# Performance work log

Measured on AMD Instinct MI355X. Metric: run time of the kernel, lower is better.

The kernel has to match this reference:

```python
import jax, jax.numpy as jnp
import numpy as np

B, C, H, W = 4, 128, 64, 64
CQK = C // 8


def setup_inputs() -> dict:
    key = jax.random.key(0)
    ks = jax.random.split(key, 8)
    s = 0.02
    return {
        "x": jax.random.normal(ks[0], (B, C, H, W), dtype=jnp.float32),
        "Wq": jax.random.normal(ks[1], (CQK, C), dtype=jnp.float32) * s,
        "bq": jnp.zeros((CQK,), dtype=jnp.float32),
        "Wk": jax.random.normal(ks[2], (CQK, C), dtype=jnp.float32) * s,
        "bk": jnp.zeros((CQK,), dtype=jnp.float32),
        "Wv": jax.random.normal(ks[3], (C, C), dtype=jnp.float32) * s,
        "bv": jnp.zeros((C,), dtype=jnp.float32),
        "gamma": jnp.zeros((1,), dtype=jnp.float32),
    }


def reference(x, Wq, bq, Wk, bk, Wv, bv, gamma):
    b, c, h, w = x.shape
    xf = x.reshape(b, c, h * w)                      # [b, c, n]
    # 1x1 convs == per-position channel matmuls
    q = jnp.einsum('dc,bcn->bdn', Wq, xf) + bq[None, :, None]   # [b, c/8, n]
    k = jnp.einsum('dc,bcn->bdn', Wk, xf) + bk[None, :, None]   # [b, c/8, n]
    v = jnp.einsum('ec,bcn->ben', Wv, xf) + bv[None, :, None]   # [b, c, n]
    energy = jnp.einsum('bdi,bdj->bij', q, k)        # [b, n, n]
    attn = jax.nn.softmax(energy, axis=-1)           # softmax over keys j
    out = jnp.einsum('bcj,bij->bci', v, attn)        # [b, c, n]
    out = out.reshape(b, c, h, w)
    return gamma[0] * out + x
```

## Files before the change

### kernel.cpp

```cpp
#include <hip/hip_runtime.h>
#include <hip/hip_bf16.h>


#define BN 4
#define CC 128
#define NN 4096
#define DQK 16
#define KVB 64

typedef float f32x16 __attribute__((ext_vector_type(16)));
typedef short s16x8 __attribute__((ext_vector_type(8)));
typedef unsigned short u16;

union FragU { unsigned u[4]; s16x8 v; };

#if defined(__has_builtin)
#  if __has_builtin(__builtin_amdgcn_permlane32_swap)
#    define PLSWAP 1
#  endif
#endif

__device__ inline u16 to_bf16(float f) {
  unsigned u = __builtin_bit_cast(unsigned, f);
  unsigned r = u + 0x7fffu + ((u >> 16) & 1u);
  return (u16)(r >> 16);
}
__device__ inline unsigned cvt_pk(float lo, float hi) {
  unsigned r;
  asm("v_cvt_pk_bf16_f32 %0, %1, %2" : "=v"(r) : "v"(lo), "v"(hi));
  return r;
}
__device__ inline float bf16lo_f(unsigned u) {
  return __builtin_bit_cast(float, u << 16);
}
__device__ inline float bf16hi_f(unsigned u) {
  return __builtin_bit_cast(float, u & 0xffff0000u);
}

__device__ inline void half_swap(unsigned& a, unsigned& b) {
#ifdef PLSWAP
  auto r = __builtin_amdgcn_permlane32_swap(a, b, false, false);
  a = r[0]; b = r[1];
#else
  unsigned xa = (unsigned)__shfl_xor((int)a, 32);
  unsigned xb = (unsigned)__shfl_xor((int)b, 32);
  bool hi = (threadIdx.x & 32) != 0;
  unsigned na = hi ? xb : a;
  unsigned nb = hi ? b : xa;
  a = na; b = nb;
#endif
}
__device__ inline float max_partner(float t) {
#ifdef PLSWAP
  unsigned u = __builtin_bit_cast(unsigned, t);
  auto r = __builtin_amdgcn_permlane32_swap(u, u, false, false);
  return fmaxf(__builtin_bit_cast(float, r[0]), __builtin_bit_cast(float, r[1]));
#else
  return fmaxf(t, __shfl_xor(t, 32));
#endif
}
__device__ inline float add_partner(float t) {
#ifdef PLSWAP
  unsigned u = __builtin_bit_cast(unsigned, t);
  auto r = __builtin_amdgcn_permlane32_swap(u, u, false, false);
  return __builtin_bit_cast(float, r[0]) + __builtin_bit_cast(float, r[1]);
#else
  return t + __shfl_xor(t, 32);
#endif
}

__global__ __launch_bounds__(640) void proj_kernel(
    const float* __restrict__ x,
    const float* __restrict__ Wq, const float* __restrict__ bq,
    const float* __restrict__ Wk, const float* __restrict__ bk,
    const float* __restrict__ Wv, const float* __restrict__ bv,
    u16* __restrict__ Qt, u16* __restrict__ Kt, u16* __restrict__ Vb)
{
  __shared__ float xs[CC][64];
  __shared__ u16 vout[CC][64];
  __shared__ u16 qkout[2][32][32];
  const int tid = threadIdx.x;
  const int wave = tid >> 6;
  const int lane = tid & 63;
  const int l31 = lane & 31, h = lane >> 5;
  const int b = blockIdx.x >> 6;
  const int n0 = (blockIdx.x & 63) << 6;

  const float* xb = x + ((size_t)b * CC) * NN + n0;
  #pragma unroll
  for (int k = 0; k < 4; ++k) {
    int id = tid + 640 * k;
    if (id < 2048) {
      int c = id >> 4, f = (id & 15) * 4;
      *reinterpret_cast<float4*>(&xs[c][f]) =
          *reinterpret_cast<const float4*>(xb + (size_t)c * NN + f);
    }
  }
  __syncthreads();

  const int nh = wave & 1, at = wave >> 1;
  const int nc = nh * 32 + l31;

  s16x8 bx[8];
  #pragma unroll
  for (int ks = 0; ks < 8; ++ks) {
    FragU f;
    #pragma unroll
    for (int q = 0; q < 4; ++q) {
      int c = 16 * ks + 8 * h + 2 * q;
      f.u[q] = cvt_pk(xs[c][nc], xs[c + 1][nc]);
    }
    bx[ks] = f.v;
  }

  f32x16 acc;
  #pragma unroll
  for (int r = 0; r < 16; ++r) acc[r] = 0.f;

  const float LOG2E = 1.44269504088896340736f;

  const float* wrow;
  if (at == 0)
    wrow = (l31 < 16) ? (Wq + (size_t)l31 * CC) : (Wk + (size_t)(l31 - 16) * CC);
  else
    wrow = Wv + (size_t)((at - 1) * 32 + l31) * CC;

  #pragma unroll
  for (int ks = 0; ks < 8; ++ks) {
    const float* wp = wrow + 16 * ks + 8 * h;
    float4 w0 = *reinterpret_cast<const float4*>(wp);
    float4 w1 = *reinterpret_cast<const float4*>(wp + 4);
    FragU a;
    a.u[0] = cvt_pk(w0.x, w0.y); a.u[1] = cvt_pk(w0.z, w0.w);
    a.u[2] = cvt_pk(w1.x, w1.y); a.u[3] = cvt_pk(w1.z, w1.w);
    acc = __builtin_amdgcn_mfma_f32_32x32x16_bf16(a.v, bx[ks], acc, 0, 0, 0);
  }

  if (at == 0) {
    #pragma unroll
    for (int r = 0; r < 16; ++r) {
      int row = (r & 3) + 8 * (r >> 2) + 4 * h;
      float val = acc[r];
      val = (row < 16) ? (val + bq[row]) * LOG2E : (val + bk[row - 16]);
      qkout[nh][row][l31] = to_bf16(val);
    }
  } else {
    #pragma unroll
    for (int r = 0; r < 16; ++r) {
      int e = (at - 1) * 32 + (r & 3) + 8 * (r >> 2) + 4 * h;
      vout[e][nh * 32 + l31] = to_bf16(acc[r] + bv[e]);
    }
  }
  __syncthreads();

  for (int id = tid; id < 1024; id += 640) {
    int isK = id >> 9, j = id & 511;
    int ni = j >> 3, ch = j & 7;
    int nhh = ni >> 5, n32 = ni & 31;
    unsigned lo = qkout[nhh][isK * 16 + 2 * ch][n32];
    unsigned hi = qkout[nhh][isK * 16 + 2 * ch + 1][n32];
    u16* dst = (isK ? Kt : Qt) + ((size_t)b * NN + n0 + ni) * DQK + 2 * ch;
    *reinterpret_cast<unsigned*>(dst) = lo | (hi << 16);
  }
  for (int id = tid; id < 1024; id += 640) {
    int c = id >> 3, q16 = id & 7;
    s16x8 v = *reinterpret_cast<const s16x8*>(&vout[c][q16 * 8]);
    *reinterpret_cast<s16x8*>(Vb + ((size_t)b * CC + c) * NN + n0 + q16 * 8) = v;
  }
}

__global__ __launch_bounds__(512, 4) void flash_kernel(
    const u16* __restrict__ Qt, const u16* __restrict__ Kt,
    const u16* __restrict__ Vb,
    unsigned* __restrict__ Opart, float* __restrict__ mstat,
    float* __restrict__ lstat, int JS)
{
  __shared__ u16 Vs[2][CC * KVB];
  __shared__ u16 Ks[2][KVB * DQK];
  const int tid = threadIdx.x;
  const int wv = tid >> 6;
  const int lane = tid & 63;
  const int l31 = lane & 31, h = lane >> 5;
  const int qb = blockIdx.x & 15;
  const int bs = blockIdx.x >> 4;
  const int b = bs / JS, sg = bs % JS;
  const int i0 = qb * 256 + wv * 32;
  const int seglen = NN / JS;
  const int j_begin = sg * seglen;
  const int niter = seglen / KVB;

  const int sc0 = tid >> 3;
  const int so = (tid & 7) * 16;
  const int sw0 = (sc0 & 7) << 4;

  const u16* Kb = Kt + (size_t)b * NN * DQK;
  const u16* Vbb = Vb + (size_t)b * CC * NN;

  const int kp_row = tid >> 1, kp_half = tid & 1;
  const int kp_slot = kp_row * DQK + ((kp_half ^ (kp_row & 1)) << 3);

  s16x8 qf = *reinterpret_cast<const s16x8*>(
      Qt + ((size_t)b * NN + i0 + l31) * DQK + 8 * h);

  f32x16 zero;
  #pragma unroll
  for (int r = 0; r < 16; ++r) zero[r] = 0.f;
  f32x16 acc[4];
  #pragma unroll
  for (int ct = 0; ct < 4; ++ct) acc[ct] = zero;
  float m_run = -__builtin_inff();
  float l_run = 0.f;

  {
    s16x8 g0 = *reinterpret_cast<const s16x8*>(
        Vbb + (size_t)sc0 * NN + j_begin + so / 2);
    s16x8 g1 = *reinterpret_cast<const s16x8*>(
        Vbb + (size_t)(64 + sc0) * NN + j_begin + so / 2);
    *reinterpret_cast<s16x8*>(&Vs[0][sc0 * KVB + ((so ^ sw0) >> 1)]) = g0;
    *reinterpret_cast<s16x8*>(&Vs[0][(64 + sc0) * KVB + ((so ^ sw0) >> 1)]) = g1;
    if (tid < 128) {
      s16x8 gk = *reinterpret_cast<const s16x8*>(
          Kb + (size_t)j_begin * DQK + tid * 8);
      *reinterpret_cast<s16x8*>(&Ks[0][kp_slot]) = gk;
    }
  }
  __syncthreads();

  const int rsw = (l31 & 7) << 4;
  const int kr0 = l31 * DQK + ((h ^ (l31 & 1)) << 3);
  const int kr1 = (32 + l31) * DQK + ((h ^ (l31 & 1)) << 3);

  for (int t = 0; t < niter; ++t) {
    const int cur = t & 1;
    s16x8 g0, g1, gk;
    const bool more = (t + 1 < niter);
    if (more) {
      const int jn = j_begin + (t + 1) * KVB;
      g0 = *reinterpret_cast<const s16x8*>(
          Vbb + (size_t)sc0 * NN + jn + so / 2);
      g1 = *reinterpret_cast<const s16x8*>(
          Vbb + (size_t)(64 + sc0) * NN + jn + so / 2);
      if (tid < 128)
        gk = *reinterpret_cast<const s16x8*>(
            Kb + (size_t)jn * DQK + tid * 8);
    }

    s16x8 kf0 = *reinterpret_cast<const s16x8*>(&Ks[cur][kr0]);
    s16x8 kf1 = *reinterpret_cast<const s16x8*>(&Ks[cur][kr1]);

    #pragma unroll
    for (int s = 0; s < 2; ++s) {
      f32x16 sv = __builtin_amdgcn_mfma_f32_32x32x16_bf16(
          s ? kf1 : kf0, qf, zero, 0, 0, 0);

      float t0 = fmaxf(fmaxf(sv[0], sv[1]), sv[2]);
      float t1 = fmaxf(fmaxf(sv[3], sv[4]), sv[5]);
      float t2 = fmaxf(fmaxf(sv[6], sv[7]), sv[8]);
      float t3 = fmaxf(fmaxf(sv[9], sv[10]), sv[11]);
      float t4 = fmaxf(fmaxf(sv[12], sv[13]), sv[14]);
      float u0 = fmaxf(fmaxf(t0, t1), t2);
      float u1 = fmaxf(fmaxf(t3, t4), sv[15]);
      float cmb = max_partner(fmaxf(u0, u1));
      float m_new = (cmb > m_run + 8.f) ? cmb : m_run;
      if (__any(m_new > m_run)) {
        float alpha = __builtin_amdgcn_exp2f(m_run - m_new);
        l_run *= alpha;
        #pragma unroll
        for (int ct = 0; ct < 4; ++ct)
          #pragma unroll
          for (int r = 0; r < 16; ++r) acc[ct][r] *= alpha;
        m_run = m_new;
      }

      float p[16];
      #pragma unroll
      for (int r = 0; r < 16; ++r)
        p[r] = __builtin_amdgcn_exp2f(sv[r] - m_run);
      float s01 = p[0] + p[1],  s23 = p[2] + p[3];
      float s45 = p[4] + p[5],  s67 = p[6] + p[7];
      float s89 = p[8] + p[9],  sab = p[10] + p[11];
      float scd = p[12] + p[13], sef = p[14] + p[15];
      l_run += ((s01 + s23) + (s45 + s67)) + ((s89 + sab) + (scd + sef));

      unsigned w0_ = cvt_pk(p[0], p[1]),  w1_ = cvt_pk(p[2], p[3]);
      unsigned w2_ = cvt_pk(p[4], p[5]),  w3_ = cvt_pk(p[6], p[7]);
      unsigned w4_ = cvt_pk(p[8], p[9]),  w5_ = cvt_pk(p[10], p[11]);
      unsigned w6_ = cvt_pk(p[12], p[13]), w7_ = cvt_pk(p[14], p[15]);
      half_swap(w0_, w2_);
      half_swap(w1_, w3_);
      half_swap(w4_, w6_);
      half_swap(w5_, w7_);
      FragU f0, f1;
      f0.u[0] = w0_; f0.u[1] = w1_; f0.u[2] = w2_; f0.u[3] = w3_;
      f1.u[0] = w4_; f1.u[1] = w5_; f1.u[2] = w6_; f1.u[3] = w7_;

      #pragma unroll
      for (int ct = 0; ct < 4; ++ct) {
        const int c = 32 * ct + l31;
        s16x8 va = *reinterpret_cast<const s16x8*>(
            &Vs[cur][c * KVB + (((s * 64 + h * 16) ^ rsw) >> 1)]);
        s16x8 vb2 = *reinterpret_cast<const s16x8*>(
            &Vs[cur][c * KVB + (((s * 64 + 32 + h * 16) ^ rsw) >> 1)]);
        acc[ct] = __builtin_amdgcn_mfma_f32_32x32x16_bf16(va, f0.v,
                                                          acc[ct], 0, 0, 0);
        acc[ct] = __builtin_amdgcn_mfma_f32_32x32x16_bf16(vb2, f1.v,
                                                          acc[ct], 0, 0, 0);
      }
    }

    if (more) {
      *reinterpret_cast<s16x8*>(
          &Vs[cur ^ 1][sc0 * KVB + ((so ^ sw0) >> 1)]) = g0;
      *reinterpret_cast<s16x8*>(
          &Vs[cur ^ 1][(64 + sc0) * KVB + ((so ^ sw0) >> 1)]) = g1;
      if (tid < 128)
        *reinterpret_cast<s16x8*>(&Ks[cur ^ 1][kp_slot]) = gk;
    }
    __syncthreads();
  }

  float l_tot = add_partner(l_run);

  unsigned* Ob = Opart + ((size_t)(b * JS + sg) * 64) * NN;
  #pragma unroll
  for (int ct = 0; ct < 4; ++ct)
    #pragma unroll
    for (int q = 0; q < 8; ++q) {
      unsigned pv = cvt_pk(acc[ct][2 * q], acc[ct][2 * q + 1]);
      int c = 32 * ct + ((2 * q) & 3) + 8 * (q >> 1) + 4 * h;
      Ob[(size_t)(c >> 1) * NN + i0 + l31] = pv;
    }
  if (lane < 32) {
    mstat[((size_t)(b * JS + sg)) * NN + i0 + l31] = m_run;
    lstat[((size_t)(b * JS + sg)) * NN + i0 + l31] = l_tot;
  }
}

template <int JS>
__global__ __launch_bounds__(256) void merge_kernel(
    const unsigned* __restrict__ Opart, const float* __restrict__ mstat,
    const float* __restrict__ lstat, const float* __restrict__ x,
    const float* __restrict__ gamma, float* __restrict__ out)
{
  const int tid = threadIdx.x;
  const int il = tid & 63;
  const int cg = tid >> 6;
  const int bid = blockIdx.x;
  const int b = bid >> 8;
  const int rem = bid & 255;
  const int i = (((rem >> 3) << 6) + il) * 2;
  const int c2 = ((rem & 7) * 4 + cg) * 2;

  float m0 = -__builtin_inff(), m1 = m0;
  float ms0[JS], ms1[JS];
  #pragma unroll
  for (int s = 0; s < JS; ++s) {
    const float* mp = mstat + ((size_t)(b * JS + s)) * NN + i;
    ms0[s] = mp[0]; ms1[s] = mp[1];
    m0 = fmaxf(m0, ms0[s]); m1 = fmaxf(m1, ms1[s]);
  }
  float d0 = 0.f, d1 = 0.f;
  float w0[JS], w1[JS];
  #pragma unroll
  for (int s = 0; s < JS; ++s) {
    const float* lp = lstat + ((size_t)(b * JS + s)) * NN + i;
    w0[s] = __builtin_amdgcn_exp2f(ms0[s] - m0);
    w1[s] = __builtin_amdgcn_exp2f(ms1[s] - m1);
    d0 += w0[s] * lp[0];
    d1 += w1[s] * lp[1];
  }
  const float g = gamma[0];
  const float g0 = g / d0, g1 = g / d1;
  #pragma unroll
  for (int s = 0; s < JS; ++s) { w0[s] *= g0; w1[s] *= g1; }

  float o[4][2] = {{0.f, 0.f}, {0.f, 0.f}, {0.f, 0.f}, {0.f, 0.f}};
  #pragma unroll
  for (int s = 0; s < JS; ++s) {
    const unsigned* Ob = Opart + ((size_t)(b * JS + s) * 64) * NN;
    uint2 A = *reinterpret_cast<const uint2*>(&Ob[(size_t)c2 * NN + i]);
    uint2 Bv = *reinterpret_cast<const uint2*>(&Ob[(size_t)(c2 + 1) * NN + i]);
    o[0][0] += w0[s] * bf16lo_f(A.x);  o[1][0] += w0[s] * bf16hi_f(A.x);
    o[0][1] += w1[s] * bf16lo_f(A.y);  o[1][1] += w1[s] * bf16hi_f(A.y);
    o[2][0] += w0[s] * bf16lo_f(Bv.x); o[3][0] += w0[s] * bf16hi_f(Bv.x);
    o[2][1] += w1[s] * bf16lo_f(Bv.y); o[3][1] += w1[s] * bf16hi_f(Bv.y);
  }
  #pragma unroll
  for (int cc = 0; cc < 4; ++cc) {
    size_t oidx = ((size_t)b * CC + 2 * c2 + cc) * NN + i;
    float2 xv = *reinterpret_cast<const float2*>(x + oidx);
    float2 ov; ov.x = o[cc][0] + xv.x; ov.y = o[cc][1] + xv.y;
    *reinterpret_cast<float2*>(out + oidx) = ov;
  }
}

extern "C" void kernel_launch(void* const* d_in, const int* in_sizes, int n_in,
                              void* d_out, int out_size, void* d_ws,
                              size_t ws_size, hipStream_t stream)
{
  const float* x     = (const float*)d_in[0];
  const float* Wq    = (const float*)d_in[1];
  const float* bq    = (const float*)d_in[2];
  const float* Wk    = (const float*)d_in[3];
  const float* bk    = (const float*)d_in[4];
  const float* Wv    = (const float*)d_in[5];
  const float* bv    = (const float*)d_in[6];
  const float* gamma = (const float*)d_in[7];
  float* out = (float*)d_out;

  char* wsb = (char*)d_ws;
  const size_t szQ = (size_t)BN * NN * DQK * 2;
  const size_t szV = (size_t)BN * CC * NN * 2;
  const size_t base = 2 * szQ + szV;
  auto need = [&](size_t js) {
    return base + js * ((size_t)2 * BN * NN * 4 + (size_t)BN * 64 * NN * 4);
  };
  int JS = 8;
  if (ws_size < need(8)) JS = 4;
  if (ws_size < need(4)) JS = 2;
  if (ws_size < need(2)) JS = 1;

  u16* Qt = (u16*)(wsb);
  u16* Kt = (u16*)(wsb + szQ);
  u16* Vb = (u16*)(wsb + 2 * szQ);
  float* mstat = (float*)(wsb + base);
  float* lstat = (float*)(wsb + base + (size_t)JS * BN * NN * 4);
  unsigned* Opart = (unsigned*)(wsb + base + (size_t)2 * JS * BN * NN * 4);

  proj_kernel<<<dim3(BN * 64), dim3(640), 0, stream>>>(
      x, Wq, bq, Wk, bk, Wv, bv, Qt, Kt, Vb);
  flash_kernel<<<dim3(BN * 16 * JS), dim3(512), 0, stream>>>(
      Qt, Kt, Vb, Opart, mstat, lstat, JS);
  if (JS == 8)
    merge_kernel<8><<<dim3(BN * 256), dim3(256), 0, stream>>>(
        Opart, mstat, lstat, x, gamma, out);
  else if (JS == 4)
    merge_kernel<4><<<dim3(BN * 256), dim3(256), 0, stream>>>(
        Opart, mstat, lstat, x, gamma, out);
  else if (JS == 2)
    merge_kernel<2><<<dim3(BN * 256), dim3(256), 0, stream>>>(
        Opart, mstat, lstat, x, gamma, out);
  else
    merge_kernel<1><<<dim3(BN * 256), dim3(256), 0, stream>>>(
        Opart, mstat, lstat, x, gamma, out);
}
```

Before: 116.7 us.

## Shrink flash blocks to 4 waves and raise MFMA wave priority

The flash attention kernel now uses 256-thread blocks covering 128 queries each instead of 512 threads covering 256, doubling the grid. Each thread loads four V rows per tile instead of two. s_setprio is raised around the MFMA sections so matrix work is prioritised over other waves. The aim is finer scheduling granularity and better overlap, but each K/V tile loaded into LDS is now shared by half as many queries, doubling global and LDS staging traffic per query.

Measured after the change: 123.0 us. 5.4% more time.

```diff
diff --git a/kernel.cpp b/kernel.cpp
--- a/kernel.cpp
+++ b/kernel.cpp
@@ -169,7 +169,7 @@
   }
 }
 
-__global__ __launch_bounds__(512, 4) void flash_kernel(
+__global__ __launch_bounds__(256, 4) void flash_kernel(
     const u16* __restrict__ Qt, const u16* __restrict__ Kt,
     const u16* __restrict__ Vb,
     unsigned* __restrict__ Opart, float* __restrict__ mstat,
@@ -181,18 +181,14 @@
   const int wv = tid >> 6;
   const int lane = tid & 63;
   const int l31 = lane & 31, h = lane >> 5;
-  const int qb = blockIdx.x & 15;
-  const int bs = blockIdx.x >> 4;
+  const int qb = blockIdx.x & 31;
+  const int bs = blockIdx.x >> 5;
   const int b = bs / JS, sg = bs % JS;
-  const int i0 = qb * 256 + wv * 32;
+  const int i0 = qb * 128 + wv * 32;
   const int seglen = NN / JS;
   const int j_begin = sg * seglen;
   const int niter = seglen / KVB;
 
-  const int sc0 = tid >> 3;
-  const int so = (tid & 7) * 16;
-  const int sw0 = (sc0 & 7) << 4;
-
   const u16* Kb = Kt + (size_t)b * NN * DQK;
   const u16* Vbb = Vb + (size_t)b * CC * NN;
 
@@ -212,12 +208,15 @@
   float l_run = 0.f;
 
   {
-    s16x8 g0 = *reinterpret_cast<const s16x8*>(
-        Vbb + (size_t)sc0 * NN + j_begin + so / 2);
-    s16x8 g1 = *reinterpret_cast<const s16x8*>(
-        Vbb + (size_t)(64 + sc0) * NN + j_begin + so / 2);
-    *reinterpret_cast<s16x8*>(&Vs[0][sc0 * KVB + ((so ^ sw0) >> 1)]) = g0;
-    *reinterpret_cast<s16x8*>(&Vs[0][(64 + sc0) * KVB + ((so ^ sw0) >> 1)]) = g1;
+    #pragma unroll
+    for (int k = 0; k < 4; ++k) {
+      int id = tid + 256 * k;
+      int row = id >> 3, q = id & 7;
+      s16x8 g = *reinterpret_cast<const s16x8*>(
+          Vbb + (size_t)row * NN + j_begin + q * 8);
+      *reinterpret_cast<s16x8*>(
+          &Vs[0][row * KVB + (((q * 16) ^ ((row & 7) << 4)) >> 1)]) = g;
+    }
     if (tid < 128) {
       s16x8 gk = *reinterpret_cast<const s16x8*>(
           Kb + (size_t)j_begin * DQK + tid * 8);
@@ -232,14 +231,15 @@
 
   for (int t = 0; t < niter; ++t) {
     const int cur = t & 1;
-    s16x8 g0, g1, gk;
+    s16x8 g0, g1, g2, g3, gk;
     const bool more = (t + 1 < niter);
     if (more) {
       const int jn = j_begin + (t + 1) * KVB;
-      g0 = *reinterpret_cast<const s16x8*>(
-          Vbb + (size_t)sc0 * NN + jn + so / 2);
-      g1 = *reinterpret_cast<const s16x8*>(
-          Vbb + (size_t)(64 + sc0) * NN + jn + so / 2);
+      const int r0 = tid >> 3, q0 = (tid & 7) * 8;
+      g0 = *reinterpret_cast<const s16x8*>(Vbb + (size_t)r0 * NN + jn + q0);
+      g1 = *reinterpret_cast<const s16x8*>(Vbb + (size_t)(32 + r0) * NN + jn + q0);
+      g2 = *reinterpret_cast<const s16x8*>(Vbb + (size_t)(64 + r0) * NN + jn + q0);
+      g3 = *reinterpret_cast<const s16x8*>(Vbb + (size_t)(96 + r0) * NN + jn + q0);
       if (tid < 128)
         gk = *reinterpret_cast<const s16x8*>(
             Kb + (size_t)jn * DQK + tid * 8);
@@ -250,8 +250,10 @@
 
     #pragma unroll
     for (int s = 0; s < 2; ++s) {
+      __builtin_amdgcn_s_setprio(1);
       f32x16 sv = __builtin_amdgcn_mfma_f32_32x32x16_bf16(
           s ? kf1 : kf0, qf, zero, 0, 0, 0);
+      __builtin_amdgcn_s_setprio(0);
 
       float t0 = fmaxf(fmaxf(sv[0], sv[1]), sv[2]);
       float t1 = fmaxf(fmaxf(sv[3], sv[4]), sv[5]);
@@ -294,6 +296,7 @@
       f0.u[0] = w0_; f0.u[1] = w1_; f0.u[2] = w2_; f0.u[3] = w3_;
       f1.u[0] = w4_; f1.u[1] = w5_; f1.u[2] = w6_; f1.u[3] = w7_;
 
+      __builtin_amdgcn_s_setprio(1);
       #pragma unroll
       for (int ct = 0; ct < 4; ++ct) {
         const int c = 32 * ct + l31;
@@ -306,13 +309,20 @@
         acc[ct] = __builtin_amdgcn_mfma_f32_32x32x16_bf16(vb2, f1.v,
                                                           acc[ct], 0, 0, 0);
       }
+      __builtin_amdgcn_s_setprio(0);
     }
 
     if (more) {
+      const int r0 = tid >> 3;
+      const int sl = ((tid & 7) * 16);
       *reinterpret_cast<s16x8*>(
-          &Vs[cur ^ 1][sc0 * KVB + ((so ^ sw0) >> 1)]) = g0;
+          &Vs[cur ^ 1][r0 * KVB + ((sl ^ ((r0 & 7) << 4)) >> 1)]) = g0;
       *reinterpret_cast<s16x8*>(
-          &Vs[cur ^ 1][(64 + sc0) * KVB + ((so ^ sw0) >> 1)]) = g1;
+          &Vs[cur ^ 1][(32 + r0) * KVB + ((sl ^ ((r0 & 7) << 4)) >> 1)]) = g1;
+      *reinterpret_cast<s16x8*>(
+          &Vs[cur ^ 1][(64 + r0) * KVB + ((sl ^ ((r0 & 7) << 4)) >> 1)]) = g2;
+      *reinterpret_cast<s16x8*>(
+          &Vs[cur ^ 1][(96 + r0) * KVB + ((sl ^ ((r0 & 7) << 4)) >> 1)]) = g3;
       if (tid < 128)
         *reinterpret_cast<s16x8*>(&Ks[cur ^ 1][kp_slot]) = gk;
     }
@@ -429,7 +439,7 @@
 
   proj_kernel<<<dim3(BN * 64), dim3(640), 0, stream>>>(
       x, Wq, bq, Wk, bk, Wv, bv, Qt, Kt, Vb);
-  flash_kernel<<<dim3(BN * 16 * JS), dim3(512), 0, stream>>>(
+  flash_kernel<<<dim3(BN * 32 * JS), dim3(256), 0, stream>>>(
       Qt, Kt, Vb, Opart, mstat, lstat, JS);
   if (JS == 8)
     merge_kernel<8><<<dim3(BN * 256), dim3(256), 0, stream>>>(
```
